# Kernel tuning notes

Hardware: AMD Instinct MI355X
Metric: run time of the kernel (lower is better)

## Reference

```python
import jax, jax.numpy as jnp
import numpy as np

STRIDE = 1
PAD = 1
DIL = 1


def setup_inputs() -> dict:
    key = jax.random.key(0)
    k1, k2, k3, k4, k5 = jax.random.split(key, 5)
    B, Cin, D, H, W = 1, 32, 16, 56, 56
    Cout, K = 64, 27  # 3x3x3 kernel
    x = jax.random.normal(k1, (B, Cin, D, H, W), jnp.float32)
    # offset-predicting conv: 3*offset_groups*K output channels (dz,dy,dx per kernel pt)
    # (module inits these to zero; we use small random values to exercise interpolation)
    offset_w = jax.random.normal(k2, (3 * K, Cin, 3, 3, 3), jnp.float32) * 0.02
    offset_b = jax.random.normal(k3, (3 * K,), jnp.float32) * 0.02
    weight = jax.random.normal(k4, (Cout, Cin, 3, 3, 3), jnp.float32) / np.sqrt(Cin * K).astype(np.float32)
    bias = jax.random.normal(k5, (Cout,), jnp.float32) * 0.01
    return {"x": x, "offset_w": offset_w, "offset_b": offset_b, "weight": weight, "bias": bias}


def _trilinear_sample(xc, coords):
    # xc: [C, D, H, W]; coords: [K, P, 3] float (z, y, x) in input voxel space.
    # Zero padding outside bounds (torchvision deform_conv convention).
    C, D, H, W = xc.shape
    xf = xc.reshape(C, D * H * W)
    z, y, x = coords[..., 0], coords[..., 1], coords[..., 2]
    z0, y0, x0 = jnp.floor(z), jnp.floor(y), jnp.floor(x)
    fz, fy, fx = z - z0, y - y0, x - x0
    acc = jnp.zeros((C,) + z.shape, xc.dtype)
    for dz in (0, 1):
        wz = fz if dz else 1.0 - fz
        zi = z0 + dz
        for dy in (0, 1):
            wy = fy if dy else 1.0 - fy
            yi = y0 + dy
            for dx in (0, 1):
                wx = fx if dx else 1.0 - fx
                xi = x0 + dx
                valid = (zi >= 0) & (zi < D) & (yi >= 0) & (yi < H) & (xi >= 0) & (xi < W)
                idx = ((jnp.clip(zi, 0, D - 1) * H + jnp.clip(yi, 0, H - 1)) * W
                       + jnp.clip(xi, 0, W - 1)).astype(jnp.int32)
                w = (wz * wy * wx) * valid.astype(xc.dtype)
                acc = acc + w[None] * xf[:, idx]  # gather -> [C, K, P]
    return acc


def _forward(x, offset_w, offset_b, weight, bias):
    B, Cin, D, H, W = x.shape
    Cout = weight.shape[0]
    kd, kh, kw = weight.shape[2:]
    K = kd * kh * kw
    # dense Conv3d predicting offsets: [B, 3K, Do, Ho, Wo]
    off = jax.lax.conv_general_dilated(
        x, offset_w, (STRIDE,) * 3, [(PAD, PAD)] * 3, rhs_dilation=(DIL,) * 3,
        dimension_numbers=("NCDHW", "OIDHW", "NCDHW")) + offset_b[None, :, None, None, None]
    Do, Ho, Wo = off.shape[2:]
    P = Do * Ho * Wo
    off = off.reshape(B, K, 3, P).transpose(0, 1, 3, 2)  # [B, K, P, 3] (dz,dy,dx)
    # base sampling grid per kernel point
    kz, ky, kx = jnp.meshgrid(jnp.arange(kd), jnp.arange(kh), jnp.arange(kw), indexing="ij")
    kz, ky, kx = kz.reshape(K), ky.reshape(K), kx.reshape(K)
    gz, gy, gx = jnp.meshgrid(jnp.arange(Do) * STRIDE - PAD,
                              jnp.arange(Ho) * STRIDE - PAD,
                              jnp.arange(Wo) * STRIDE - PAD, indexing="ij")
    pz = (kz * DIL)[:, None] + gz.reshape(-1)[None]  # [K, P]
    py = (ky * DIL)[:, None] + gy.reshape(-1)[None]
    px = (kx * DIL)[:, None] + gx.reshape(-1)[None]
    base = jnp.stack([pz, py, px], axis=-1).astype(off.dtype)  # [K, P, 3]
    coords = off + base[None]  # [B, K, P, 3]
    sampled = jax.vmap(_trilinear_sample)(x, coords)  # [B, Cin, K, P]
    out = jnp.einsum("bckp,ock->bop", sampled, weight.reshape(Cout, Cin, K)) + bias[None, :, None]
    return out.reshape(B, Cout, Do, Ho, Wo)


def reference(x, offset_w, offset_b, weight, bias):
    return _forward(x, offset_w, offset_b, weight, bias)
```

## Files before the change

kernel.cpp:

```cpp
#include <hip/hip_runtime.h>
#include <math.h>

#define D_   16
#define H_   56
#define W_   56
#define CIN  32
#define COUT 64
#define KPTS 27
#define NCH  81
#define NP   (D_*H_*W_)
#define CHW  (D_*H_*W_)
#define KPAD 28

typedef float f4 __attribute__((ext_vector_type(4)));

static __device__ __forceinline__ int iclamp(int v, int lo, int hi) {
    return v < lo ? lo : (v > hi ? hi : v);
}

__global__ __launch_bounds__(256) void k_prep(const float* __restrict__ w,
                                              const float* __restrict__ ow,
                                              float* __restrict__ wT,
                                              float* __restrict__ owT) {
    int i = blockIdx.x * 256 + threadIdx.x;
    if (i < COUT * CIN * KPTS) {
        int tap = i % KPTS;
        int c   = (i / KPTS) % CIN;
        int o   = i / (KPTS * CIN);
        wT[(tap * CIN + c) * COUT + o] = w[i];
    }
    if (i < NCH * CIN * KPTS) {
        int tap = i % KPTS;
        int c   = (i / KPTS) % CIN;
        int ch  = i / (KPTS * CIN);
        int d   = ch % 3;
        int kpt = ch / 3;
        owT[(((tap * 3) + d) * CIN + c) * KPAD + kpt] = ow[i];
    }
    if (i < KPTS * 3 * CIN)
        owT[i * KPAD + 27] = 0.0f;
}

__global__ __launch_bounds__(64) void k_xT(const float* __restrict__ x,
                                           float* __restrict__ xT) {
    const int s = blockIdx.x * 64 + threadIdx.x;
    float r[CIN];
#pragma unroll
    for (int c = 0; c < CIN; ++c) r[c] = x[c * CHW + s];
    f4* dst = (f4*)(xT + (size_t)s * CIN);
#pragma unroll
    for (int cc = 0; cc < 8; ++cc) {
        f4 v;
        v.x = r[cc * 4 + 0]; v.y = r[cc * 4 + 1];
        v.z = r[cc * 4 + 2]; v.w = r[cc * 4 + 3];
        dst[cc] = v;
    }
}

__global__ __launch_bounds__(256) void k_init(const float* __restrict__ bias,
                                              float* __restrict__ out) {
    const int i   = blockIdx.x * 256 + threadIdx.x;
    const float b = bias[(i * 4) / NP];
    f4 v; v.x = b; v.y = b; v.z = b; v.w = b;
    ((f4*)out)[i] = v;
}

__global__ __launch_bounds__(64, 2) void k_offsets(const float* __restrict__ xT,
                                                   const float* __restrict__ owT,
                                                   const float* __restrict__ offb,
                                                   float* __restrict__ coords) {
    const int tid = threadIdx.x;
    const int p   = blockIdx.x * 64 + tid;
    const int d   = blockIdx.y;
    const int ox  = p % W_;
    const int t   = p / W_;
    const int oy  = t % H_;
    const int oz  = t / H_;

    f4 A0, A1, A2, A3, A4, A5, A6;
#define INIT4(Ai, kb) { f4 v; \
    v.x = offb[((kb) + 0) * 3 + d]; \
    v.y = offb[((kb) + 1) * 3 + d]; \
    v.z = offb[((kb) + 2) * 3 + d]; \
    v.w = ((kb) + 3 < KPTS) ? offb[((kb) + 3) * 3 + d] : 0.0f; \
    Ai = v; }
    INIT4(A0, 0) INIT4(A1, 4) INIT4(A2, 8) INIT4(A3, 12)
    INIT4(A4, 16) INIT4(A5, 20) INIT4(A6, 24)
#undef INIT4

    for (int tap = 0; tap < KPTS; ++tap) {
        const int kz = tap / 9, ky = (tap / 3) % 3, kx = tap % 3;
        const int zi = oz - 1 + kz, yi = oy - 1 + ky, xi = ox - 1 + kx;
        const bool val = ((unsigned)zi < (unsigned)D_) &&
                         ((unsigned)yi < (unsigned)H_) &&
                         ((unsigned)xi < (unsigned)W_);
        const int zc = iclamp(zi, 0, D_ - 1);
        const int yc = iclamp(yi, 0, H_ - 1);
        const int xc = iclamp(xi, 0, W_ - 1);
        const float m = val ? 1.0f : 0.0f;
        const f4* src = (const f4*)(xT + (size_t)((zc * H_ + yc) * W_ + xc) * CIN);

        f4 X0 = src[0] * m, X1 = src[1] * m, X2 = src[2] * m, X3 = src[3] * m;
        f4 X4 = src[4] * m, X5 = src[5] * m, X6 = src[6] * m, X7 = src[7] * m;

        const f4* w4 = (const f4*)(owT + (size_t)((tap * 3 + d) * CIN) * KPAD);
#define OF(xs, cfull) { const float s_ = (xs); const f4* wp = w4 + (cfull) * 7; \
    A0 += wp[0] * s_; A1 += wp[1] * s_; A2 += wp[2] * s_; A3 += wp[3] * s_; \
    A4 += wp[4] * s_; A5 += wp[5] * s_; A6 += wp[6] * s_; }
#define OCC(Xi, cc) { OF(Xi.x, (cc)*4+0) OF(Xi.y, (cc)*4+1) \
                      OF(Xi.z, (cc)*4+2) OF(Xi.w, (cc)*4+3) }
        OCC(X0, 0) OCC(X1, 1) OCC(X2, 2) OCC(X3, 3)
        OCC(X4, 4) OCC(X5, 5) OCC(X6, 6) OCC(X7, 7)
#undef OCC
#undef OF
    }

#define BASEF(kk) ((d == 0) ? (float)(oz - 1 + (kk) / 9) \
                 : (d == 1) ? (float)(oy - 1 + ((kk) / 3) % 3) \
                            : (float)(ox - 1 + (kk) % 3))
#define WOUT(Ai, kb) { \
    coords[(d * KPTS + (kb) + 0) * NP + p] = Ai.x + BASEF((kb) + 0); \
    coords[(d * KPTS + (kb) + 1) * NP + p] = Ai.y + BASEF((kb) + 1); \
    coords[(d * KPTS + (kb) + 2) * NP + p] = Ai.z + BASEF((kb) + 2); \
    if ((kb) + 3 < KPTS) \
        coords[(d * KPTS + (kb) + 3) * NP + p] = Ai.w + BASEF((kb) + 3); }
    WOUT(A0, 0) WOUT(A1, 4) WOUT(A2, 8) WOUT(A3, 12)
    WOUT(A4, 16) WOUT(A5, 20) WOUT(A6, 24)
#undef WOUT
#undef BASEF
}

__global__ __launch_bounds__(64, 2) void k_dconv(const float* __restrict__ xT,
                                                 const float* __restrict__ coords,
                                                 const float* __restrict__ wT,
                                                 float* __restrict__ out) {
    const int tid = threadIdx.x;
    const int p   = blockIdx.x * 64 + tid;
    const int g   = blockIdx.y;

    f4 A0 = 0, A1 = 0, A2 = 0, A3 = 0, A4 = 0, A5 = 0, A6 = 0, A7 = 0;
    f4 A8 = 0, A9 = 0, A10 = 0, A11 = 0, A12 = 0, A13 = 0, A14 = 0, A15 = 0;

    for (int tap = 9 * g; tap < 9 * g + 9; ++tap) {
        const float cz = coords[(0 * KPTS + tap) * NP + p];
        const float cy = coords[(1 * KPTS + tap) * NP + p];
        const float cx = coords[(2 * KPTS + tap) * NP + p];

        const float zf = floorf(cz), yf = floorf(cy), xf = floorf(cx);
        const float fz = cz - zf, fy = cy - yf, fx = cx - xf;
        const int z0 = (int)zf, y0 = (int)yf, x0 = (int)xf;

        float cw0, cw1, cw2, cw3, cw4, cw5, cw6, cw7;
        int   cb0, cb1, cb2, cb3, cb4, cb5, cb6, cb7;
#define CORNER(jj, Wj, Bj) { \
    const int dz_ = (jj) >> 2, dy_ = ((jj) >> 1) & 1, dx_ = (jj) & 1; \
    const int zi_ = z0 + dz_, yi_ = y0 + dy_, xi_ = x0 + dx_; \
    const bool v_ = ((unsigned)zi_ < (unsigned)D_) && \
                    ((unsigned)yi_ < (unsigned)H_) && \
                    ((unsigned)xi_ < (unsigned)W_); \
    const float wz_ = dz_ ? fz : 1.0f - fz; \
    const float wy_ = dy_ ? fy : 1.0f - fy; \
    const float wx_ = dx_ ? fx : 1.0f - fx; \
    Wj = v_ ? wz_ * wy_ * wx_ : 0.0f; \
    Bj = ((iclamp(zi_, 0, D_ - 1) * H_ + iclamp(yi_, 0, H_ - 1)) * W_ \
          + iclamp(xi_, 0, W_ - 1)) * CIN; }
        CORNER(0, cw0, cb0) CORNER(1, cw1, cb1) CORNER(2, cw2, cb2)
        CORNER(3, cw3, cb3) CORNER(4, cw4, cb4) CORNER(5, cw5, cb5)
        CORNER(6, cw6, cb6) CORNER(7, cw7, cb7)
#undef CORNER

        const f4* w4 = (const f4*)(wT + (size_t)tap * CIN * COUT);
#define LDX(Bj, cc) (*(const f4*)(xT + (Bj) + (cc) * 4))
#define SFMA(sv, eidx, cc) { const float s_ = (sv); \
    const f4* wq = w4 + (((cc) * 4 + (eidx)) * 16); \
    A0  += wq[0]  * s_; A1  += wq[1]  * s_; A2  += wq[2]  * s_; A3  += wq[3]  * s_; \
    A4  += wq[4]  * s_; A5  += wq[5]  * s_; A6  += wq[6]  * s_; A7  += wq[7]  * s_; \
    A8  += wq[8]  * s_; A9  += wq[9]  * s_; A10 += wq[10] * s_; A11 += wq[11] * s_; \
    A12 += wq[12] * s_; A13 += wq[13] * s_; A14 += wq[14] * s_; A15 += wq[15] * s_; }
#define CCBLK(cc) { \
    f4 s = cw0 * LDX(cb0, cc); \
    s += cw1 * LDX(cb1, cc);  s += cw2 * LDX(cb2, cc); \
    s += cw3 * LDX(cb3, cc);  s += cw4 * LDX(cb4, cc); \
    s += cw5 * LDX(cb5, cc);  s += cw6 * LDX(cb6, cc); \
    s += cw7 * LDX(cb7, cc); \
    SFMA(s.x, 0, cc) SFMA(s.y, 1, cc) SFMA(s.z, 2, cc) SFMA(s.w, 3, cc) }
        CCBLK(0) CCBLK(1) CCBLK(2) CCBLK(3)
        CCBLK(4) CCBLK(5) CCBLK(6) CCBLK(7)
#undef CCBLK
#undef SFMA
#undef LDX
    }

    float* op = out + p;
#define AOUT(Ai, ob) { \
    atomicAdd(op + ((ob) + 0) * NP, Ai.x); atomicAdd(op + ((ob) + 1) * NP, Ai.y); \
    atomicAdd(op + ((ob) + 2) * NP, Ai.z); atomicAdd(op + ((ob) + 3) * NP, Ai.w); }
    AOUT(A0, 0)  AOUT(A1, 4)  AOUT(A2, 8)   AOUT(A3, 12)
    AOUT(A4, 16) AOUT(A5, 20) AOUT(A6, 24)  AOUT(A7, 28)
    AOUT(A8, 32) AOUT(A9, 36) AOUT(A10, 40) AOUT(A11, 44)
    AOUT(A12, 48) AOUT(A13, 52) AOUT(A14, 56) AOUT(A15, 60)
#undef AOUT
}

extern "C" void kernel_launch(void* const* d_in, const int* in_sizes, int n_in,
                              void* d_out, int out_size, void* d_ws, size_t ws_size,
                              hipStream_t stream) {
    const float* x    = (const float*)d_in[0];
    const float* offw = (const float*)d_in[1];
    const float* offb = (const float*)d_in[2];
    const float* wgt  = (const float*)d_in[3];
    const float* bias = (const float*)d_in[4];
    float* out = (float*)d_out;

    float* ws     = (float*)d_ws;
    float* coords = ws;
    float* wT     = coords + 3 * KPTS * NP;
    float* owT    = wT + KPTS * CIN * COUT;
    float* xT     = owT + KPTS * 3 * CIN * KPAD;

    const int n_tr = NCH * CIN * KPTS;
    hipLaunchKernelGGL(k_prep, dim3((n_tr + 255) / 256), dim3(256), 0, stream,
                       wgt, offw, wT, owT);
    hipLaunchKernelGGL(k_xT, dim3(NP / 64), dim3(64), 0, stream, x, xT);
    hipLaunchKernelGGL(k_init, dim3(COUT * NP / 4 / 256), dim3(256), 0, stream,
                       bias, out);
    hipLaunchKernelGGL(k_offsets, dim3(NP / 64, 3), dim3(64), 0, stream,
                       xT, owT, offb, coords);
    hipLaunchKernelGGL(k_dconv, dim3(NP / 64, 3), dim3(64), 0, stream,
                       xT, coords, wT, out);
}
```

Before: 559.8 us.

## Split offset conv by tap group and dconv by output-channel half for occupancy

The offset-prediction kernel is now split over three tap groups per coordinate dimension. A separate init kernel writes bias plus base grid into coords, and the partial sums are combined with atomicAdd. The deformable conv kernel is split into two output-channel halves of 32, which halves the accumulator registers, and launch bounds are raised to 4 blocks per CU. The aim is more parallel blocks and more resident waves; the cost is extra atomics, an extra init pass, and sampling done twice (once per channel half).

After: 578.3 us. 3.3% more time.

```diff
diff --git a/kernel.cpp b/kernel.cpp
--- a/kernel.cpp
+++ b/kernel.cpp
@@ -65,30 +65,39 @@
     ((f4*)out)[i] = v;
 }
 
-__global__ __launch_bounds__(64, 2) void k_offsets(const float* __restrict__ xT,
+__global__ __launch_bounds__(256) void k_init_coords(const float* __restrict__ offb,
+                                                     float* __restrict__ coords) {
+    const int i  = blockIdx.x * 256 + threadIdx.x;
+    const int p  = i % NP;
+    const int ck = i / NP;
+    const int d  = ck / KPTS;
+    const int k  = ck % KPTS;
+    const int kz = k / 9, ky = (k / 3) % 3, kx = k % 3;
+    const int x  = p % W_;
+    const int y  = (p / W_) % H_;
+    const int z  = p / (W_ * H_);
+    const float base = (d == 0) ? (float)(z - 1 + kz)
+                     : (d == 1) ? (float)(y - 1 + ky)
+                                : (float)(x - 1 + kx);
+    coords[i] = offb[k * 3 + d] + base;
+}
+
+__global__ __launch_bounds__(64, 4) void k_offsets(const float* __restrict__ xT,
                                                    const float* __restrict__ owT,
-                                                   const float* __restrict__ offb,
                                                    float* __restrict__ coords) {
     const int tid = threadIdx.x;
     const int p   = blockIdx.x * 64 + tid;
-    const int d   = blockIdx.y;
+    const int by  = blockIdx.y;
+    const int d   = by / 3;
+    const int tg  = by % 3;
     const int ox  = p % W_;
     const int t   = p / W_;
     const int oy  = t % H_;
     const int oz  = t / H_;
 
-    f4 A0, A1, A2, A3, A4, A5, A6;
-#define INIT4(Ai, kb) { f4 v; \
-    v.x = offb[((kb) + 0) * 3 + d]; \
-    v.y = offb[((kb) + 1) * 3 + d]; \
-    v.z = offb[((kb) + 2) * 3 + d]; \
-    v.w = ((kb) + 3 < KPTS) ? offb[((kb) + 3) * 3 + d] : 0.0f; \
-    Ai = v; }
-    INIT4(A0, 0) INIT4(A1, 4) INIT4(A2, 8) INIT4(A3, 12)
-    INIT4(A4, 16) INIT4(A5, 20) INIT4(A6, 24)
-#undef INIT4
-
-    for (int tap = 0; tap < KPTS; ++tap) {
+    f4 A0 = 0, A1 = 0, A2 = 0, A3 = 0, A4 = 0, A5 = 0, A6 = 0;
+
+    for (int tap = 9 * tg; tap < 9 * tg + 9; ++tap) {
         const int kz = tap / 9, ky = (tap / 3) % 3, kx = tap % 3;
         const int zi = oz - 1 + kz, yi = oy - 1 + ky, xi = ox - 1 + kx;
         const bool val = ((unsigned)zi < (unsigned)D_) &&
@@ -115,33 +124,30 @@
 #undef OF
     }
 
-#define BASEF(kk) ((d == 0) ? (float)(oz - 1 + (kk) / 9) \
-                 : (d == 1) ? (float)(oy - 1 + ((kk) / 3) % 3) \
-                            : (float)(ox - 1 + (kk) % 3))
-#define WOUT(Ai, kb) { \
-    coords[(d * KPTS + (kb) + 0) * NP + p] = Ai.x + BASEF((kb) + 0); \
-    coords[(d * KPTS + (kb) + 1) * NP + p] = Ai.y + BASEF((kb) + 1); \
-    coords[(d * KPTS + (kb) + 2) * NP + p] = Ai.z + BASEF((kb) + 2); \
-    if ((kb) + 3 < KPTS) \
-        coords[(d * KPTS + (kb) + 3) * NP + p] = Ai.w + BASEF((kb) + 3); }
-    WOUT(A0, 0) WOUT(A1, 4) WOUT(A2, 8) WOUT(A3, 12)
-    WOUT(A4, 16) WOUT(A5, 20) WOUT(A6, 24)
-#undef WOUT
-#undef BASEF
-}
-
-__global__ __launch_bounds__(64, 2) void k_dconv(const float* __restrict__ xT,
+    float* cp = coords + (size_t)d * KPTS * NP + p;
+#define COUTA(Ai, kb) { \
+    atomicAdd(cp + ((kb) + 0) * NP, Ai.x); \
+    atomicAdd(cp + ((kb) + 1) * NP, Ai.y); \
+    atomicAdd(cp + ((kb) + 2) * NP, Ai.z); \
+    if ((kb) + 3 < KPTS) atomicAdd(cp + ((kb) + 3) * NP, Ai.w); }
+    COUTA(A0, 0) COUTA(A1, 4) COUTA(A2, 8) COUTA(A3, 12)
+    COUTA(A4, 16) COUTA(A5, 20) COUTA(A6, 24)
+#undef COUTA
+}
+
+__global__ __launch_bounds__(64, 4) void k_dconv(const float* __restrict__ xT,
                                                  const float* __restrict__ coords,
                                                  const float* __restrict__ wT,
                                                  float* __restrict__ out) {
     const int tid = threadIdx.x;
     const int p   = blockIdx.x * 64 + tid;
-    const int g   = blockIdx.y;
+    const int by  = blockIdx.y;
+    const int og  = by & 1;
+    const int tg  = by >> 1;
 
     f4 A0 = 0, A1 = 0, A2 = 0, A3 = 0, A4 = 0, A5 = 0, A6 = 0, A7 = 0;
-    f4 A8 = 0, A9 = 0, A10 = 0, A11 = 0, A12 = 0, A13 = 0, A14 = 0, A15 = 0;
-
-    for (int tap = 9 * g; tap < 9 * g + 9; ++tap) {
+
+    for (int tap = 9 * tg; tap < 9 * tg + 9; ++tap) {
         const float cz = coords[(0 * KPTS + tap) * NP + p];
         const float cy = coords[(1 * KPTS + tap) * NP + p];
         const float cx = coords[(2 * KPTS + tap) * NP + p];
@@ -169,14 +175,12 @@
         CORNER(6, cw6, cb6) CORNER(7, cw7, cb7)
 #undef CORNER
 
-        const f4* w4 = (const f4*)(wT + (size_t)tap * CIN * COUT);
+        const f4* w4 = (const f4*)(wT + (size_t)tap * CIN * COUT + og * 32);
 #define LDX(Bj, cc) (*(const f4*)(xT + (Bj) + (cc) * 4))
 #define SFMA(sv, eidx, cc) { const float s_ = (sv); \
     const f4* wq = w4 + (((cc) * 4 + (eidx)) * 16); \
-    A0  += wq[0]  * s_; A1  += wq[1]  * s_; A2  += wq[2]  * s_; A3  += wq[3]  * s_; \
-    A4  += wq[4]  * s_; A5  += wq[5]  * s_; A6  += wq[6]  * s_; A7  += wq[7]  * s_; \
-    A8  += wq[8]  * s_; A9  += wq[9]  * s_; A10 += wq[10] * s_; A11 += wq[11] * s_; \
-    A12 += wq[12] * s_; A13 += wq[13] * s_; A14 += wq[14] * s_; A15 += wq[15] * s_; }
+    A0 += wq[0] * s_; A1 += wq[1] * s_; A2 += wq[2] * s_; A3 += wq[3] * s_; \
+    A4 += wq[4] * s_; A5 += wq[5] * s_; A6 += wq[6] * s_; A7 += wq[7] * s_; }
 #define CCBLK(cc) { \
     f4 s = cw0 * LDX(cb0, cc); \
     s += cw1 * LDX(cb1, cc);  s += cw2 * LDX(cb2, cc); \
@@ -191,14 +195,12 @@
 #undef LDX
     }
 
-    float* op = out + p;
+    float* op = out + (size_t)og * 32 * NP + p;
 #define AOUT(Ai, ob) { \
     atomicAdd(op + ((ob) + 0) * NP, Ai.x); atomicAdd(op + ((ob) + 1) * NP, Ai.y); \
     atomicAdd(op + ((ob) + 2) * NP, Ai.z); atomicAdd(op + ((ob) + 3) * NP, Ai.w); }
-    AOUT(A0, 0)  AOUT(A1, 4)  AOUT(A2, 8)   AOUT(A3, 12)
-    AOUT(A4, 16) AOUT(A5, 20) AOUT(A6, 24)  AOUT(A7, 28)
-    AOUT(A8, 32) AOUT(A9, 36) AOUT(A10, 40) AOUT(A11, 44)
-    AOUT(A12, 48) AOUT(A13, 52) AOUT(A14, 56) AOUT(A15, 60)
+    AOUT(A0, 0)  AOUT(A1, 4)  AOUT(A2, 8)  AOUT(A3, 12)
+    AOUT(A4, 16) AOUT(A5, 20) AOUT(A6, 24) AOUT(A7, 28)
 #undef AOUT
 }
 
@@ -224,8 +226,10 @@
     hipLaunchKernelGGL(k_xT, dim3(NP / 64), dim3(64), 0, stream, x, xT);
     hipLaunchKernelGGL(k_init, dim3(COUT * NP / 4 / 256), dim3(256), 0, stream,
                        bias, out);
-    hipLaunchKernelGGL(k_offsets, dim3(NP / 64, 3), dim3(64), 0, stream,
-                       xT, owT, offb, coords);
-    hipLaunchKernelGGL(k_dconv, dim3(NP / 64, 3), dim3(64), 0, stream,
+    hipLaunchKernelGGL(k_init_coords, dim3(NCH * NP / 256), dim3(256), 0, stream,
+                       offb, coords);
+    hipLaunchKernelGGL(k_offsets, dim3(NP / 64, 9), dim3(64), 0, stream,
+                       xT, owT, coords);
+    hipLaunchKernelGGL(k_dconv, dim3(NP / 64, 6), dim3(64), 0, stream,
                        xT, coords, wT, out);
 }
```

## Drop channel-last transpose and gather directly from NCDHW input

Applied to the files above, without the earlier changes.

Removes the k_xT kernel that transposed x into a channel-last layout. k_offsets and k_dconv now read x in its original channel-planar layout, one scalar per channel, inside a partially unrolled channel loop. This saves one launch and the transpose's read and write traffic. In exchange, every corner gather becomes 32 scattered scalar loads instead of 8 contiguous vector loads per voxel. That likely lowers cache-line efficiency in the dominant sampling kernel.

After: 583.9 us. +4.3%, slower.

```diff
diff --git a/kernel.cpp b/kernel.cpp
--- a/kernel.cpp
+++ b/kernel.cpp
@@ -41,22 +41,6 @@
         owT[i * KPAD + 27] = 0.0f;
 }
 
-__global__ __launch_bounds__(64) void k_xT(const float* __restrict__ x,
-                                           float* __restrict__ xT) {
-    const int s = blockIdx.x * 64 + threadIdx.x;
-    float r[CIN];
-#pragma unroll
-    for (int c = 0; c < CIN; ++c) r[c] = x[c * CHW + s];
-    f4* dst = (f4*)(xT + (size_t)s * CIN);
-#pragma unroll
-    for (int cc = 0; cc < 8; ++cc) {
-        f4 v;
-        v.x = r[cc * 4 + 0]; v.y = r[cc * 4 + 1];
-        v.z = r[cc * 4 + 2]; v.w = r[cc * 4 + 3];
-        dst[cc] = v;
-    }
-}
-
 __global__ __launch_bounds__(256) void k_init(const float* __restrict__ bias,
                                               float* __restrict__ out) {
     const int i   = blockIdx.x * 256 + threadIdx.x;
@@ -65,7 +49,7 @@
     ((f4*)out)[i] = v;
 }
 
-__global__ __launch_bounds__(64, 2) void k_offsets(const float* __restrict__ xT,
+__global__ __launch_bounds__(64, 2) void k_offsets(const float* __restrict__ x,
                                                    const float* __restrict__ owT,
                                                    const float* __restrict__ offb,
                                                    float* __restrict__ coords) {
@@ -94,25 +78,19 @@
         const bool val = ((unsigned)zi < (unsigned)D_) &&
                          ((unsigned)yi < (unsigned)H_) &&
                          ((unsigned)xi < (unsigned)W_);
-        const int zc = iclamp(zi, 0, D_ - 1);
-        const int yc = iclamp(yi, 0, H_ - 1);
-        const int xc = iclamp(xi, 0, W_ - 1);
+        const int sidx = (iclamp(zi, 0, D_ - 1) * H_ + iclamp(yi, 0, H_ - 1)) * W_
+                       + iclamp(xi, 0, W_ - 1);
         const float m = val ? 1.0f : 0.0f;
-        const f4* src = (const f4*)(xT + (size_t)((zc * H_ + yc) * W_ + xc) * CIN);
-
-        f4 X0 = src[0] * m, X1 = src[1] * m, X2 = src[2] * m, X3 = src[3] * m;
-        f4 X4 = src[4] * m, X5 = src[5] * m, X6 = src[6] * m, X7 = src[7] * m;
 
         const f4* w4 = (const f4*)(owT + (size_t)((tap * 3 + d) * CIN) * KPAD);
-#define OF(xs, cfull) { const float s_ = (xs); const f4* wp = w4 + (cfull) * 7; \
-    A0 += wp[0] * s_; A1 += wp[1] * s_; A2 += wp[2] * s_; A3 += wp[3] * s_; \
-    A4 += wp[4] * s_; A5 += wp[5] * s_; A6 += wp[6] * s_; }
-#define OCC(Xi, cc) { OF(Xi.x, (cc)*4+0) OF(Xi.y, (cc)*4+1) \
-                      OF(Xi.z, (cc)*4+2) OF(Xi.w, (cc)*4+3) }
-        OCC(X0, 0) OCC(X1, 1) OCC(X2, 2) OCC(X3, 3)
-        OCC(X4, 4) OCC(X5, 5) OCC(X6, 6) OCC(X7, 7)
-#undef OCC
-#undef OF
+#pragma unroll 4
+        for (int c = 0; c < CIN; ++c) {
+            const float xv = m * x[c * CHW + sidx];
+            const f4* wp = w4 + c * 7;
+            A0 += wp[0] * xv; A1 += wp[1] * xv; A2 += wp[2] * xv;
+            A3 += wp[3] * xv; A4 += wp[4] * xv; A5 += wp[5] * xv;
+            A6 += wp[6] * xv;
+        }
     }
 
 #define BASEF(kk) ((d == 0) ? (float)(oz - 1 + (kk) / 9) \
@@ -130,7 +108,7 @@
 #undef BASEF
 }
 
-__global__ __launch_bounds__(64, 2) void k_dconv(const float* __restrict__ xT,
+__global__ __launch_bounds__(64, 2) void k_dconv(const float* __restrict__ x,
                                                  const float* __restrict__ coords,
                                                  const float* __restrict__ wT,
                                                  float* __restrict__ out) {
@@ -162,33 +140,27 @@
     const float wy_ = dy_ ? fy : 1.0f - fy; \
     const float wx_ = dx_ ? fx : 1.0f - fx; \
     Wj = v_ ? wz_ * wy_ * wx_ : 0.0f; \
-    Bj = ((iclamp(zi_, 0, D_ - 1) * H_ + iclamp(yi_, 0, H_ - 1)) * W_ \
-          + iclamp(xi_, 0, W_ - 1)) * CIN; }
+    Bj = (iclamp(zi_, 0, D_ - 1) * H_ + iclamp(yi_, 0, H_ - 1)) * W_ \
+         + iclamp(xi_, 0, W_ - 1); }
         CORNER(0, cw0, cb0) CORNER(1, cw1, cb1) CORNER(2, cw2, cb2)
         CORNER(3, cw3, cb3) CORNER(4, cw4, cb4) CORNER(5, cw5, cb5)
         CORNER(6, cw6, cb6) CORNER(7, cw7, cb7)
 #undef CORNER
 
-        const f4* w4 = (const f4*)(wT + (size_t)tap * CIN * COUT);
-#define LDX(Bj, cc) (*(const f4*)(xT + (Bj) + (cc) * 4))
-#define SFMA(sv, eidx, cc) { const float s_ = (sv); \
-    const f4* wq = w4 + (((cc) * 4 + (eidx)) * 16); \
-    A0  += wq[0]  * s_; A1  += wq[1]  * s_; A2  += wq[2]  * s_; A3  += wq[3]  * s_; \
-    A4  += wq[4]  * s_; A5  += wq[5]  * s_; A6  += wq[6]  * s_; A7  += wq[7]  * s_; \
-    A8  += wq[8]  * s_; A9  += wq[9]  * s_; A10 += wq[10] * s_; A11 += wq[11] * s_; \
-    A12 += wq[12] * s_; A13 += wq[13] * s_; A14 += wq[14] * s_; A15 += wq[15] * s_; }
-#define CCBLK(cc) { \
-    f4 s = cw0 * LDX(cb0, cc); \
-    s += cw1 * LDX(cb1, cc);  s += cw2 * LDX(cb2, cc); \
-    s += cw3 * LDX(cb3, cc);  s += cw4 * LDX(cb4, cc); \
-    s += cw5 * LDX(cb5, cc);  s += cw6 * LDX(cb6, cc); \
-    s += cw7 * LDX(cb7, cc); \
-    SFMA(s.x, 0, cc) SFMA(s.y, 1, cc) SFMA(s.z, 2, cc) SFMA(s.w, 3, cc) }
-        CCBLK(0) CCBLK(1) CCBLK(2) CCBLK(3)
-        CCBLK(4) CCBLK(5) CCBLK(6) CCBLK(7)
-#undef CCBLK
-#undef SFMA
-#undef LDX
+        const float* wtap = wT + (size_t)tap * CIN * COUT;
+#pragma unroll 4
+        for (int c = 0; c < CIN; ++c) {
+            const float* xc = x + c * CHW;
+            const float v0 = xc[cb0], v1 = xc[cb1], v2 = xc[cb2], v3 = xc[cb3];
+            const float v4 = xc[cb4], v5 = xc[cb5], v6 = xc[cb6], v7 = xc[cb7];
+            const float s = cw0 * v0 + cw1 * v1 + cw2 * v2 + cw3 * v3
+                          + cw4 * v4 + cw5 * v5 + cw6 * v6 + cw7 * v7;
+            const f4* wq = (const f4*)(wtap + c * COUT);
+            A0  += wq[0]  * s; A1  += wq[1]  * s; A2  += wq[2]  * s; A3  += wq[3]  * s;
+            A4  += wq[4]  * s; A5  += wq[5]  * s; A6  += wq[6]  * s; A7  += wq[7]  * s;
+            A8  += wq[8]  * s; A9  += wq[9]  * s; A10 += wq[10] * s; A11 += wq[11] * s;
+            A12 += wq[12] * s; A13 += wq[13] * s; A14 += wq[14] * s; A15 += wq[15] * s;
+        }
     }
 
     float* op = out + p;
@@ -216,16 +188,14 @@
     float* coords = ws;
     float* wT     = coords + 3 * KPTS * NP;
     float* owT    = wT + KPTS * CIN * COUT;
-    float* xT     = owT + KPTS * 3 * CIN * KPAD;
 
     const int n_tr = NCH * CIN * KPTS;
     hipLaunchKernelGGL(k_prep, dim3((n_tr + 255) / 256), dim3(256), 0, stream,
                        wgt, offw, wT, owT);
-    hipLaunchKernelGGL(k_xT, dim3(NP / 64), dim3(64), 0, stream, x, xT);
     hipLaunchKernelGGL(k_init, dim3(COUT * NP / 4 / 256), dim3(256), 0, stream,
                        bias, out);
     hipLaunchKernelGGL(k_offsets, dim3(NP / 64, 3), dim3(64), 0, stream,
-                       xT, owT, offb, coords);
+                       x, owT, offb, coords);
     hipLaunchKernelGGL(k_dconv, dim3(NP / 64, 3), dim3(64), 0, stream,
-                       xT, coords, wT, out);
-}
+                       x, coords, wT, out);
+}
```
